# Optimization experiments

Hardware: AMD Instinct MI355X
Metric: run time of the kernel (lower is better)

Reference implementation:

```python
import jax, jax.numpy as jnp
import numpy as np

DIM = 768
HEAD_DIM = 64          # num_head arg (per-head dim)
N_HEADS = DIM // HEAD_DIM  # 12
B, N = 4, 2048


def setup_inputs() -> dict:
    key = jax.random.key(0)
    ks = jax.random.split(key, 7)
    s = DIM ** -0.5
    return {
        "x":  jax.random.normal(ks[0], (B, N, DIM), jnp.float32),
        "wq": jax.random.normal(ks[1], (DIM, DIM), jnp.float32) * s,
        "bq": jax.random.normal(ks[2], (DIM,), jnp.float32) * 0.01,
        "wk": jax.random.normal(ks[3], (DIM, DIM), jnp.float32) * s,
        "bk": jax.random.normal(ks[4], (DIM,), jnp.float32) * 0.01,
        "wv": jax.random.normal(ks[5], (DIM, DIM), jnp.float32) * s,
        "bv": jax.random.normal(ks[6], (DIM,), jnp.float32) * 0.01,
    }


def reference(x, wq, bq, wk, bk, wv, bv):
    # torch Linear: y = x @ W.T + b
    q = x @ wq.T + bq
    k = x @ wk.T + bk
    v = x @ wv.T + bv
    # split heads: b n (h d) -> b h n d
    def split(t):
        return t.reshape(B, N, N_HEADS, HEAD_DIM).transpose(0, 2, 1, 3)
    q, k, v = split(q), split(k), split(v)
    scale = HEAD_DIM ** -0.5
    logit = jnp.einsum("bhnd,bhmd->bhnm", q, k) * scale  # [B,H,N,N]
    attn = jax.nn.softmax(logit, axis=-1)
    out = jnp.einsum("bhnm,bhmd->bhnd", attn, v)
    # concat heads: b h n d -> b n (h d)
    return out.transpose(0, 2, 1, 3).reshape(B, N, DIM)
```

## Files before the change

kernel.cpp:

```cpp
#include <hip/hip_runtime.h>
#include <cstdint>

#define NSEQ 2048
#define DIM  768
#define NH   12
#define HD   64

typedef __attribute__((ext_vector_type(8)))  short bf16x8;
typedef __attribute__((ext_vector_type(4)))  float f32x4;
typedef __attribute__((ext_vector_type(16))) float f32x16;
typedef __attribute__((ext_vector_type(4)))  int   i32x4;
typedef unsigned short u16;

#define MFMA16(a,b,c) __builtin_amdgcn_mfma_f32_16x16x32_bf16(a,b,c,0,0,0)
#define MFMA32(a,b,c) __builtin_amdgcn_mfma_f32_32x32x16_bf16(a,b,c,0,0,0)

#define QSCALE 0.1803368801111204f

__device__ __forceinline__ u16 f2bf(float f){
  unsigned u = __builtin_bit_cast(unsigned, f);
  return (u16)((u + 0x7fffu + ((u >> 16) & 1u)) >> 16);
}
__device__ __forceinline__ int cvtpk(float a, float b){
  int r;
  asm("v_cvt_pk_bf16_f32 %0, %1, %2" : "=v"(r) : "v"(a), "v"(b));
  return r;
}

typedef __attribute__((address_space(1))) void gvoid_t;
typedef __attribute__((address_space(3))) void lvoid_t;
__device__ __forceinline__ void g2l16(const void* g, void* l){
  __builtin_amdgcn_global_load_lds((gvoid_t*)g, (lvoid_t*)l, 16, 0, 0);
}

__global__ __launch_bounds__(256) void convert_all(
    const float* __restrict__ x,  const float* __restrict__ wq,
    const float* __restrict__ wk, const float* __restrict__ wv,
    u16* __restrict__ xb, u16* __restrict__ wb){
  int blk = blockIdx.x, tid = threadIdx.x;
  const float* src; u16* dst; long idx;
  if (blk < 6144){ src = x; dst = xb; idx = (long)blk*256 + tid; }
  else {
    int r = blk - 6144; int s = r / 576; r -= s*576;
    src = (s==0) ? wq : (s==1) ? wk : wv;
    dst = wb + (long)s * (768*768);
    idx = (long)r*256 + tid;
  }
  float4 v = ((const float4*)src)[idx];
  ushort4 o;
  o.x = f2bf(v.x); o.y = f2bf(v.y); o.z = f2bf(v.z); o.w = f2bf(v.w);
  ((ushort4*)dst)[idx] = o;
}

__global__ __launch_bounds__(256,3) void qkv_gemm(
    const u16* __restrict__ xb, const u16* __restrict__ wb,
    const float* __restrict__ bq, const float* __restrict__ bk,
    const float* __restrict__ bv,
    u16* __restrict__ Qo, u16* __restrict__ Ko, u16* __restrict__ Vo){
  __shared__ __align__(16) u16 ldsX[128*64];
  __shared__ __align__(16) u16 ldsW[128*64];
  int tid  = threadIdx.x;
  int w    = tid >> 6, lane = tid & 63;
  int xcd  = blockIdx.x & 7, j = blockIdx.x >> 3;
  int bm   = xcd*8 + j/18, bn = j%18;
  int wm   = w >> 1, wn = w & 1;
  int l15  = lane & 15, g = lane >> 4;
  int srow = lane >> 3;
  int scol = ((lane & 7) ^ srow) * 8;

  const u16* xg = xb + (long)bm*128*768;
  const u16* wg = wb + (long)bn*128*768;

  f32x4 acc[4][4] = {};

  for (int k0 = 0; k0 < 768; k0 += 64){
    if (k0) __syncthreads();
    #pragma unroll
    for (int jj = 0; jj < 4; jj++){
      int rr = (w*4 + jj)*8 + srow;
      g2l16(xg + (long)rr*768 + k0 + scol, &ldsX[(w*4 + jj)*512]);
      g2l16(wg + (long)rr*768 + k0 + scol, &ldsW[(w*4 + jj)*512]);
    }
    __syncthreads();
    #pragma unroll
    for (int ks = 0; ks < 2; ks++){
      bf16x8 af[4], bfr[4];
      #pragma unroll
      for (int im = 0; im < 4; im++){
        int row = wm*64 + im*16 + l15;
        af[im] = *(const bf16x8*)&ldsX[row*64 + (((ks*4 + g) ^ (row & 7))*8)];
      }
      #pragma unroll
      for (int in = 0; in < 4; in++){
        int row = wn*64 + in*16 + l15;
        bfr[in] = *(const bf16x8*)&ldsW[row*64 + (((ks*4 + g) ^ (row & 7))*8)];
      }
      #pragma unroll
      for (int im = 0; im < 4; im++)
        #pragma unroll
        for (int in = 0; in < 4; in++)
          acc[im][in] = MFMA16(af[im], bfr[in], acc[im][in]);
    }
  }

  int seg = bn / 6;
  const float* bias = (seg==0) ? bq : (seg==1) ? bk : bv;
  #pragma unroll
  for (int in = 0; in < 4; in++){
    int o  = bn*128 + wn*64 + in*16 + l15;
    int oo = o - seg*768;
    int h  = oo >> 6, d = oo & 63;
    float bb = bias[oo];
    #pragma unroll
    for (int im = 0; im < 4; im++){
      int t  = bm*128 + wm*64 + im*16 + g*4;
      int bi = t >> 11, n0 = t & 2047;
      f32x4 a = acc[im][in];
      if (seg == 2){
        ushort4 pk;
        pk.x = f2bf(a[0] + bb); pk.y = f2bf(a[1] + bb);
        pk.z = f2bf(a[2] + bb); pk.w = f2bf(a[3] + bb);
        *(ushort4*)&Vo[((long)(bi*NH + h)*HD + d)*NSEQ + n0] = pk;
      } else if (seg == 0){
        #pragma unroll
        for (int r = 0; r < 4; r++)
          Qo[((long)(bi*NH + h)*NSEQ + n0 + r)*HD + d] = f2bf((a[r] + bb)*QSCALE);
      } else {
        #pragma unroll
        for (int r = 0; r < 4; r++)
          Ko[((long)(bi*NH + h)*NSEQ + n0 + r)*HD + d] = f2bf(a[r] + bb);
      }
    }
  }
}

__global__ __launch_bounds__(256,3) void attn(
    const u16* __restrict__ Q, const u16* __restrict__ K,
    const u16* __restrict__ VT, float* __restrict__ out){
  __shared__ __align__(16) u16 kls[2][64*64];
  __shared__ __align__(16) u16 vls[2][64*64];
  int tid = threadIdx.x;
  int w   = tid >> 6, lane = tid & 63;
  int xcd = blockIdx.x & 7, j = blockIdx.x >> 3;
  int bh  = xcd*6 + (j >> 4), qc = j & 15;
  int b   = bh / NH, h = bh - b*NH;
  int l31 = lane & 31, hi = lane >> 5;
  int srow = lane >> 3;
  int scol = ((lane & 7) ^ srow) * 8;

  const u16* Qb = Q  + (long)bh*NSEQ*HD;
  const u16* Kb = K  + (long)bh*NSEQ*HD;
  const u16* Vb = VT + (long)bh*HD*NSEQ;

  int r0 = qc*128 + w*32;
  bf16x8 qf[4];
  {
    const u16* qrow = Qb + (long)(r0 + l31)*HD;
    #pragma unroll
    for (int dk = 0; dk < 4; dk++)
      qf[dk] = *(const bf16x8*)&qrow[dk*16 + hi*8];
  }

  f32x16 oa[2] = {};
  float ls = 0.f;

#define STAGE(c0, bf)                                                         \
  {                                                                           \
    _Pragma("unroll")                                                         \
    for (int jj = 0; jj < 2; jj++){                                           \
      int rr = jj*32 + w*8;                                                   \
      g2l16(Kb + (long)((c0) + rr + srow)*HD + scol,  &kls[bf][rr*64]);       \
      g2l16(Vb + (long)(rr + srow)*NSEQ + (c0) + scol, &vls[bf][rr*64]);      \
    }                                                                         \
  }

#define KH(bf, kh)                                                            \
  {                                                                           \
    bf16x8 kf[4];                                                             \
    _Pragma("unroll")                                                         \
    for (int dk = 0; dk < 4; dk++)                                            \
      kf[dk] = *(const bf16x8*)                                               \
        &kls[bf][((kh)*32 + l31)*64 + (((dk*2 + hi) ^ (l31 & 7))*8)];         \
    f32x16 T = {};                                                            \
    __builtin_amdgcn_s_setprio(1);                                            \
    _Pragma("unroll")                                                         \
    for (int dk = 0; dk < 4; dk++)                                            \
      T = MFMA32(kf[dk], qf[dk], T);                                          \
    __builtin_amdgcn_s_setprio(0);                                            \
    int PD[4][2];                                                             \
    _Pragma("unroll")                                                         \
    for (int q = 0; q < 4; q++){                                              \
      float p0 = __builtin_amdgcn_exp2f(T[q*4+0]);                            \
      float p1 = __builtin_amdgcn_exp2f(T[q*4+1]);                            \
      float p2 = __builtin_amdgcn_exp2f(T[q*4+2]);                            \
      float p3 = __builtin_amdgcn_exp2f(T[q*4+3]);                            \
      ls += (p0 + p1) + (p2 + p3);                                            \
      PD[q][0] = cvtpk(p0, p1);                                               \
      PD[q][1] = cvtpk(p2, p3);                                               \
    }                                                                         \
    _Pragma("unroll")                                                         \
    for (int kc = 0; kc < 2; kc++){                                           \
      int a0 = PD[2*kc][0], b0 = PD[2*kc+1][0];                               \
      int a1 = PD[2*kc][1], b1 = PD[2*kc+1][1];                               \
      asm("v_permlane32_swap_b32 %0, %1" : "+v"(a0), "+v"(b0));               \
      asm("v_permlane32_swap_b32 %0, %1" : "+v"(a1), "+v"(b1));               \
      i32x4 pr;                                                               \
      pr[0] = a0; pr[1] = a1; pr[2] = b0; pr[3] = b1;                         \
      bf16x8 pf = __builtin_bit_cast(bf16x8, pr);                             \
      __builtin_amdgcn_s_setprio(1);                                          \
      _Pragma("unroll")                                                       \
      for (int dt = 0; dt < 2; dt++){                                         \
        bf16x8 vf = *(const bf16x8*)                                          \
          &vls[bf][(dt*32 + l31)*64 + ((((kh)*4 + kc*2 + hi) ^ (l31 & 7))*8)];\
        oa[dt] = MFMA32(vf, pf, oa[dt]);                                      \
      }                                                                       \
      __builtin_amdgcn_s_setprio(0);                                          \
    }                                                                         \
  }

  STAGE(0, 0);
  __syncthreads();
  for (int i = 0; i < 32; i++){
    int cb = i & 1, nb = cb ^ 1;
    STAGE(((i+1) & 31)*64, nb);
    __builtin_amdgcn_sched_barrier(0);
    asm volatile("s_waitcnt vmcnt(4) lgkmcnt(0)" ::: "memory");
    __builtin_amdgcn_sched_barrier(0);
    __builtin_amdgcn_s_barrier();
    KH(cb, 0);
    KH(cb, 1);
    __builtin_amdgcn_sched_barrier(0);
    asm volatile("s_waitcnt lgkmcnt(0)" ::: "memory");
    __builtin_amdgcn_sched_barrier(0);
    __builtin_amdgcn_s_barrier();
  }
#undef STAGE
#undef KH

  ls += __shfl_xor(ls, 32);
  float inv = 1.f / ls;

  float* op = &out[(long)(b*NSEQ + r0 + l31)*DIM + h*HD];
  #pragma unroll
  for (int dt = 0; dt < 2; dt++)
    #pragma unroll
    for (int rq = 0; rq < 4; rq++){
      f32x4 v;
      v[0] = oa[dt][rq*4+0]; v[1] = oa[dt][rq*4+1];
      v[2] = oa[dt][rq*4+2]; v[3] = oa[dt][rq*4+3];
      v *= inv;
      *(f32x4*)&op[dt*32 + rq*8 + hi*4] = v;
    }
}

extern "C" void kernel_launch(void* const* d_in, const int* in_sizes, int n_in,
                              void* d_out, int out_size, void* d_ws, size_t ws_size,
                              hipStream_t stream){
  (void)in_sizes; (void)n_in; (void)out_size; (void)ws_size;
  const float* x  = (const float*)d_in[0];
  const float* wq = (const float*)d_in[1];
  const float* bq = (const float*)d_in[2];
  const float* wk = (const float*)d_in[3];
  const float* bk = (const float*)d_in[4];
  const float* wv = (const float*)d_in[5];
  const float* bv = (const float*)d_in[6];

  char* ws = (char*)d_ws;
  u16* xb = (u16*)ws;
  u16* wb = (u16*)(ws + 12582912);
  u16* Qp = (u16*)(ws + 16121856);
  u16* Kp = (u16*)(ws + 28704768);
  u16* Vp = (u16*)(ws + 41287680);

  convert_all<<<7872, 256, 0, stream>>>(x, wq, wk, wv, xb, wb);
  qkv_gemm<<<1152, 256, 0, stream>>>(xb, wb, bq, bk, bv, Qp, Kp, Vp);
  attn<<<768, 256, 0, stream>>>(Qp, Kp, Vp, (float*)d_out);
}
```

Baseline: 191.0 us.

## Process two query tiles per wave in attention to reuse K/V fragments

Each wave of the attention kernel now handles 64 query rows as two 32-row tiles that share the K and V fragments read from LDS, so LDS reads per MFMA are halved. Blocks shrink to 128 threads (2 waves) while still covering 128 query rows, and each wave issues twice as many global-to-LDS staging loads, with the wait count adjusted to match. This raises register pressure from doubled accumulators and Q fragments, and lowers the number of waves per block available to hide latency.

```diff
diff --git a/kernel.cpp b/kernel.cpp
--- a/kernel.cpp
+++ b/kernel.cpp
@@ -134,7 +134,7 @@
   }
 }
 
-__global__ __launch_bounds__(256,3) void attn(
+__global__ __launch_bounds__(128,2) void attn(
     const u16* __restrict__ Q, const u16* __restrict__ K,
     const u16* __restrict__ VT, float* __restrict__ out){
   __shared__ __align__(16) u16 kls[2][64*64];
@@ -152,41 +152,33 @@
   const u16* Kb = K  + (long)bh*NSEQ*HD;
   const u16* Vb = VT + (long)bh*HD*NSEQ;
 
-  int r0 = qc*128 + w*32;
-  bf16x8 qf[4];
+  int r0 = qc*128 + w*64;
+  bf16x8 qfA[4], qfB[4];
   {
-    const u16* qrow = Qb + (long)(r0 + l31)*HD;
-    #pragma unroll
-    for (int dk = 0; dk < 4; dk++)
-      qf[dk] = *(const bf16x8*)&qrow[dk*16 + hi*8];
-  }
-
-  f32x16 oa[2] = {};
-  float ls = 0.f;
+    const u16* qa = Qb + (long)(r0 + l31)*HD;
+    const u16* qb2 = Qb + (long)(r0 + 32 + l31)*HD;
+    #pragma unroll
+    for (int dk = 0; dk < 4; dk++){
+      qfA[dk] = *(const bf16x8*)&qa[dk*16 + hi*8];
+      qfB[dk] = *(const bf16x8*)&qb2[dk*16 + hi*8];
+    }
+  }
+
+  f32x16 oaA[2] = {}, oaB[2] = {};
+  float lsA = 0.f, lsB = 0.f;
 
 #define STAGE(c0, bf)                                                         \
   {                                                                           \
     _Pragma("unroll")                                                         \
-    for (int jj = 0; jj < 2; jj++){                                           \
-      int rr = jj*32 + w*8;                                                   \
+    for (int jj = 0; jj < 4; jj++){                                           \
+      int rr = jj*16 + w*8;                                                   \
       g2l16(Kb + (long)((c0) + rr + srow)*HD + scol,  &kls[bf][rr*64]);       \
       g2l16(Vb + (long)(rr + srow)*NSEQ + (c0) + scol, &vls[bf][rr*64]);      \
     }                                                                         \
   }
 
-#define KH(bf, kh)                                                            \
+#define SMPV(T, vfs, oa, ls)                                                  \
   {                                                                           \
-    bf16x8 kf[4];                                                             \
-    _Pragma("unroll")                                                         \
-    for (int dk = 0; dk < 4; dk++)                                            \
-      kf[dk] = *(const bf16x8*)                                               \
-        &kls[bf][((kh)*32 + l31)*64 + (((dk*2 + hi) ^ (l31 & 7))*8)];         \
-    f32x16 T = {};                                                            \
-    __builtin_amdgcn_s_setprio(1);                                            \
-    _Pragma("unroll")                                                         \
-    for (int dk = 0; dk < 4; dk++)                                            \
-      T = MFMA32(kf[dk], qf[dk], T);                                          \
-    __builtin_amdgcn_s_setprio(0);                                            \
     int PD[4][2];                                                             \
     _Pragma("unroll")                                                         \
     for (int q = 0; q < 4; q++){                                              \
@@ -208,13 +200,43 @@
       pr[0] = a0; pr[1] = a1; pr[2] = b0; pr[3] = b1;                         \
       bf16x8 pf = __builtin_bit_cast(bf16x8, pr);                             \
       __builtin_amdgcn_s_setprio(1);                                          \
+      oa[0] = MFMA32(vfs[kc][0], pf, oa[0]);                                  \
+      oa[1] = MFMA32(vfs[kc][1], pf, oa[1]);                                  \
+      __builtin_amdgcn_s_setprio(0);                                          \
+    }                                                                         \
+  }
+
+#define KH(bf, kh)                                                            \
+  {                                                                           \
+    bf16x8 kf[4];                                                             \
+    _Pragma("unroll")                                                         \
+    for (int dk = 0; dk < 4; dk++)                                            \
+      kf[dk] = *(const bf16x8*)                                               \
+        &kls[bf][((kh)*32 + l31)*64 + (((dk*2 + hi) ^ (l31 & 7))*8)];         \
+    bf16x8 vfs[2][2];                                                         \
+    _Pragma("unroll")                                                         \
+    for (int kc = 0; kc < 2; kc++)                                            \
       _Pragma("unroll")                                                       \
-      for (int dt = 0; dt < 2; dt++){                                         \
-        bf16x8 vf = *(const bf16x8*)                                          \
+      for (int dt = 0; dt < 2; dt++)                                          \
+        vfs[kc][dt] = *(const bf16x8*)                                        \
           &vls[bf][(dt*32 + l31)*64 + ((((kh)*4 + kc*2 + hi) ^ (l31 & 7))*8)];\
-        oa[dt] = MFMA32(vf, pf, oa[dt]);                                      \
-      }                                                                       \
+    {                                                                         \
+      f32x16 T = {};                                                          \
+      __builtin_amdgcn_s_setprio(1);                                          \
+      _Pragma("unroll")                                                       \
+      for (int dk = 0; dk < 4; dk++)                                          \
+        T = MFMA32(kf[dk], qfA[dk], T);                                       \
       __builtin_amdgcn_s_setprio(0);                                          \
+      SMPV(T, vfs, oaA, lsA);                                                 \
+    }                                                                         \
+    {                                                                         \
+      f32x16 T = {};                                                          \
+      __builtin_amdgcn_s_setprio(1);                                          \
+      _Pragma("unroll")                                                       \
+      for (int dk = 0; dk < 4; dk++)                                          \
+        T = MFMA32(kf[dk], qfB[dk], T);                                       \
+      __builtin_amdgcn_s_setprio(0);                                          \
+      SMPV(T, vfs, oaB, lsB);                                                 \
     }                                                                         \
   }
 
@@ -224,7 +246,7 @@
     int cb = i & 1, nb = cb ^ 1;
     STAGE(((i+1) & 31)*64, nb);
     __builtin_amdgcn_sched_barrier(0);
-    asm volatile("s_waitcnt vmcnt(4) lgkmcnt(0)" ::: "memory");
+    asm volatile("s_waitcnt vmcnt(8) lgkmcnt(0)" ::: "memory");
     __builtin_amdgcn_sched_barrier(0);
     __builtin_amdgcn_s_barrier();
     KH(cb, 0);
@@ -236,20 +258,28 @@
   }
 #undef STAGE
 #undef KH
-
-  ls += __shfl_xor(ls, 32);
-  float inv = 1.f / ls;
-
-  float* op = &out[(long)(b*NSEQ + r0 + l31)*DIM + h*HD];
+#undef SMPV
+
+  lsA += __shfl_xor(lsA, 32);
+  lsB += __shfl_xor(lsB, 32);
+  float invA = 1.f / lsA, invB = 1.f / lsB;
+
+  float* opA = &out[(long)(b*NSEQ + r0 + l31)*DIM + h*HD];
+  float* opB = &out[(long)(b*NSEQ + r0 + 32 + l31)*DIM + h*HD];
   #pragma unroll
   for (int dt = 0; dt < 2; dt++)
     #pragma unroll
     for (int rq = 0; rq < 4; rq++){
       f32x4 v;
-      v[0] = oa[dt][rq*4+0]; v[1] = oa[dt][rq*4+1];
-      v[2] = oa[dt][rq*4+2]; v[3] = oa[dt][rq*4+3];
-      v *= inv;
-      *(f32x4*)&op[dt*32 + rq*8 + hi*4] = v;
+      v[0] = oaA[dt][rq*4+0]; v[1] = oaA[dt][rq*4+1];
+      v[2] = oaA[dt][rq*4+2]; v[3] = oaA[dt][rq*4+3];
+      v *= invA;
+      *(f32x4*)&opA[dt*32 + rq*8 + hi*4] = v;
+      f32x4 u;
+      u[0] = oaB[dt][rq*4+0]; u[1] = oaB[dt][rq*4+1];
+      u[2] = oaB[dt][rq*4+2]; u[3] = oaB[dt][rq*4+3];
+      u *= invB;
+      *(f32x4*)&opB[dt*32 + rq*8 + hi*4] = u;
     }
 }
 
@@ -274,5 +304,5 @@
 
   convert_all<<<7872, 256, 0, stream>>>(x, wq, wk, wv, xb, wb);
   qkv_gemm<<<1152, 256, 0, stream>>>(xb, wb, bq, bk, bv, Qp, Kp, Vp);
-  attn<<<768, 256, 0, stream>>>(Qp, Kp, Vp, (float*)d_out);
-}
+  attn<<<768, 128, 0, stream>>>(Qp, Kp, Vp, (float*)d_out);
+}
```

After: 202.7 us. 6.1% more time.
